# Optimization experiments

Hardware: AMD Instinct MI355X
Metric: run time of the kernel (lower is better)

The kernel has to match this reference:

```python
import jax, jax.numpy as jnp
import numpy as np

EPS = 1e-5

def _bn(x, g, b, m, v):
    # eval-mode batchnorm, NCHW, per-channel params
    inv = g / jnp.sqrt(v + EPS)
    return x * inv[None, :, None, None] + (b - m * inv)[None, :, None, None]

def setup_inputs() -> dict:
    key = jax.random.key(0)
    ks = jax.random.split(key, 16)
    C = 64
    x = jax.random.normal(ks[0], (8, C, 64, 64), dtype=jnp.float32)
    w1 = jax.random.normal(ks[1], (C, C, 1, 1), dtype=jnp.float32) * 0.1
    w2 = jax.random.normal(ks[2], (C, 1, 3, 3), dtype=jnp.float32) * 0.1
    w3 = jax.random.normal(ks[3], (C, C, 1, 1), dtype=jnp.float32) * 0.1
    def bn_params(k):
        k1, k2, k3, k4 = jax.random.split(k, 4)
        return (jax.random.uniform(k1, (C,)) + 0.5,
                jax.random.normal(k2, (C,)) * 0.1,
                jax.random.normal(k3, (C,)) * 0.1,
                jax.random.uniform(k4, (C,)) + 0.5)
    g1, b1, m1, v1 = bn_params(ks[4])
    g2, b2, m2, v2 = bn_params(ks[5])
    g3, b3, m3, v3 = bn_params(ks[6])
    return {"x": x, "w1": w1, "bn1_g": g1, "bn1_b": b1, "bn1_m": m1, "bn1_v": v1,
            "w2": w2, "bn2_g": g2, "bn2_b": b2, "bn2_m": m2, "bn2_v": v2,
            "w3": w3, "bn3_g": g3, "bn3_b": b3, "bn3_m": m3, "bn3_v": v3}

def reference(x, w1, bn1_g, bn1_b, bn1_m, bn1_v,
              w2, bn2_g, bn2_b, bn2_m, bn2_v,
              w3, bn3_g, bn3_b, bn3_m, bn3_v):
    B, c, h, w = x.shape
    N = h * w
    # conv1 (1x1) + BN + ReLU -> V
    v = jnp.einsum('bchw,oc->bohw', x, w1[:, :, 0, 0])
    v = jax.nn.relu(_bn(v, bn1_g, bn1_b, bn1_m, bn1_v))
    # attention over spatial positions: Q=K=x, single head, dim=c
    Q = x.reshape(B, c, N)          # bdn
    V = v.reshape(B, c, N)          # bdm
    scores = jnp.einsum('bdn,bdm->bnm', Q, Q) / (c ** 0.5)  # [B,N,N]
    prob = jax.nn.softmax(scores, axis=-1)
    out = jnp.einsum('bnm,bdm->bdn', prob, V).reshape(B, c, h, w)
    # depthwise conv + BN + ReLU
    out = jax.lax.conv_general_dilated(
        out, w2, window_strides=(1, 1), padding='SAME',
        dimension_numbers=('NCHW', 'OIHW', 'NCHW'), feature_group_count=c)
    out = jax.nn.relu(_bn(out, bn2_g, bn2_b, bn2_m, bn2_v))
    # pointwise conv + BN
    out = jnp.einsum('bchw,oc->bohw', out, w3[:, :, 0, 0])
    out = _bn(out, bn3_g, bn3_b, bn3_m, bn3_v)
    # residual (stride==1 and in_size==out_size)
    return out + x
```

## Files before the change

kernel.cpp:

```cpp
#include <hip/hip_runtime.h>
#include <stdint.h>

typedef __attribute__((ext_vector_type(8)))  short s16x8;
typedef __attribute__((ext_vector_type(16))) float f32x16;

union CvtI4 { int4 i; s16x8 s; };

__device__ __forceinline__ unsigned f2bf(float f) {
    union { float f; unsigned u; } v; v.f = f;
    return (v.u + 0x7fffu + ((v.u >> 16) & 1u)) >> 16;
}

__global__ __launch_bounds__(256) void k_prep(
    const float* __restrict__ x, const float* __restrict__ w1,
    const float* __restrict__ g1, const float* __restrict__ b1,
    const float* __restrict__ m1, const float* __restrict__ v1,
    unsigned short* __restrict__ xT, unsigned short* __restrict__ vbf)
{
    __shared__ float X[64 * 65];
    const int b    = blockIdx.x >> 7;
    const int n0   = ((blockIdx.x >> 1) & 63) << 6;
    const int half = blockIdx.x & 1;
    const int tid  = threadIdx.x;
    const float QS = 0.42466090014400953f;

    {
        const int r = tid >> 6, nn = tid & 63;
        const float* xb = x + (size_t)b * 262144 + n0 + nn;
#pragma unroll
        for (int cc = 0; cc < 16; ++cc) {
            int c = cc * 4 + r;
            X[c * 65 + nn] = xb[(size_t)c * 4096];
        }
    }
    __syncthreads();

    {
        const int n8 = tid >> 3, c8 = tid & 7;
        const int n = (half << 5) + n8;
        unsigned u[4];
#pragma unroll
        for (int j = 0; j < 4; ++j) {
            unsigned lo = f2bf(X[(c8 * 8 + 2 * j) * 65 + n] * QS);
            unsigned hi = f2bf(X[(c8 * 8 + 2 * j + 1) * 65 + n] * QS);
            u[j] = lo | (hi << 16);
        }
        uint4 pk; pk.x = u[0]; pk.y = u[1]; pk.z = u[2]; pk.w = u[3];
        *(uint4*)(xT + (((size_t)((b << 12) + n0 + n)) << 6) + (c8 << 3)) = pk;
    }

    {
        const int n = tid & 63, og = tid >> 6;
        float rX[64];
#pragma unroll
        for (int c = 0; c < 64; ++c) rX[c] = X[c * 65 + n];
        unsigned short* vb = vbf + (((size_t)(b << 6)) << 12) + n0 + n;
#pragma unroll 2
        for (int oo = 0; oo < 8; ++oo) {
            int o = (half << 5) + og * 8 + oo;
            float inv = g1[o] * rsqrtf(v1[o] + 1e-5f);
            float sh  = b1[o] - m1[o] * inv;
            float acc = 0.f;
#pragma unroll
            for (int c = 0; c < 64; ++c) acc = fmaf(w1[o * 64 + c], rX[c], acc);
            vb[(size_t)o << 12] = (unsigned short)f2bf(fmaxf(fmaf(acc, inv, sh), 0.f));
        }
    }
}

__global__ __launch_bounds__(256) void k_attn(
    const unsigned short* __restrict__ xT, const unsigned short* __restrict__ vbf,
    float* __restrict__ outO, float* __restrict__ outL,
    int tilesPer, int nsplit)
{
    __shared__ __align__(16) unsigned short Klds[64 * 64];
    __shared__ __align__(16) unsigned short Vlds[64 * 64];
    __shared__ __align__(16) unsigned short Plds[64 * 64];
    __shared__ float rsLds[4][32];
    __shared__ float denomT[64];

    const int xcd  = blockIdx.x & 7;
    const int slot = blockIdx.x >> 3;
    const int qgrp = slot & 63;
    const int pair = xcd * nsplit + (slot >> 6);
    const int b = pair & 7;
    const int ms = pair >> 3;

    const int tid = threadIdx.x;
    const int w = tid >> 6, lane = tid & 63;
    const int l31 = lane & 31, half = lane >> 5;
    const int qbase = qgrp << 6;

    outO += (size_t)ms * 2097152u;
    outL += (size_t)ms * 32768u;

    const int s = w & 1;
    const int t = w >> 1;

    s16x8 Bq[4];
    {
        const unsigned short* qr = xT +
            (((size_t)((b << 12) + qbase + (t << 5) + l31)) << 6) + (half << 3);
#pragma unroll
        for (int kk = 0; kk < 4; ++kk) {
            CvtI4 c; c.i = *(const int4*)(qr + (kk << 4));
            Bq[kk] = c.s;
        }
    }

    f32x16 O = {0.f,0.f,0.f,0.f,0.f,0.f,0.f,0.f,0.f,0.f,0.f,0.f,0.f,0.f,0.f,0.f};
    float rs = 0.f;
    const int mt0 = ms * tilesPer;

    for (int mt = 0; mt < tilesPer; ++mt) {
        const int m0 = (mt0 + mt) << 6;
        __syncthreads();
#pragma unroll
        for (int it = 0; it < 2; ++it) {
            int lin = (it << 8) + tid;
            {
                int km = lin >> 3, c4 = lin & 7;
                int4 d = *(const int4*)(xT + (((size_t)((b << 12) + m0 + km)) << 6) + (c4 << 3));
                *(int4*)(Klds + (km << 6) + ((c4 ^ (km & 7)) << 3)) = d;
            }
            {
                int vd = lin >> 3, c8 = lin & 7;
                int4 d = *(const int4*)(vbf + (((size_t)((b << 6) + vd)) << 12) + m0 + (c8 << 3));
                *(int4*)(Vlds + (vd << 6) + ((c8 ^ (vd & 7)) << 3)) = d;
            }
        }
        __syncthreads();

        {
            const int km = (s << 5) + l31;
            s16x8 Ak[4];
#pragma unroll
            for (int kk = 0; kk < 4; ++kk) {
                int pos = ((kk << 1) + half) ^ (km & 7);
                Ak[kk] = *(const s16x8*)(Klds + (km << 6) + (pos << 3));
            }
            f32x16 S = {0.f,0.f,0.f,0.f,0.f,0.f,0.f,0.f,0.f,0.f,0.f,0.f,0.f,0.f,0.f,0.f};
            S = __builtin_amdgcn_mfma_f32_32x32x16_bf16(Ak[0], Bq[0], S, 0, 0, 0);
            S = __builtin_amdgcn_mfma_f32_32x32x16_bf16(Ak[1], Bq[1], S, 0, 0, 0);
            S = __builtin_amdgcn_mfma_f32_32x32x16_bf16(Ak[2], Bq[2], S, 0, 0, 0);
            S = __builtin_amdgcn_mfma_f32_32x32x16_bf16(Ak[3], Bq[3], S, 0, 0, 0);

            const int nrow = (t << 5) + l31;
#pragma unroll
            for (int q = 0; q < 4; ++q) {
                float p0 = __builtin_amdgcn_exp2f(S[4*q+0]);
                float p1 = __builtin_amdgcn_exp2f(S[4*q+1]);
                float p2 = __builtin_amdgcn_exp2f(S[4*q+2]);
                float p3 = __builtin_amdgcn_exp2f(S[4*q+3]);
                rs += (p0 + p1) + (p2 + p3);
                union { float f; unsigned u; } a0, a1, a2, a3;
                a0.f = p0; a1.f = p1; a2.f = p2; a3.f = p3;
                uint2 pk;
                pk.x = ((a0.u + 0x8000u) >> 16) | ((a1.u + 0x8000u) & 0xFFFF0000u);
                pk.y = ((a2.u + 0x8000u) >> 16) | ((a3.u + 0x8000u) & 0xFFFF0000u);
                int c8 = (s << 2) + q;
                *(uint2*)(Plds + (nrow << 6) + ((c8 ^ (nrow & 7)) << 3) + (half << 2)) = pk;
            }
        }
        __syncthreads();

        {
            const int nrow = (t << 5) + l31;
            const int drow = (s << 5) + l31;
#pragma unroll
            for (int ks = 0; ks < 4; ++ks) {
                int c = (ks << 1) + half;
                const s16x8 Ap = *(const s16x8*)(Plds + (nrow << 6) + ((c ^ (nrow & 7)) << 3));
                const s16x8 Bv = *(const s16x8*)(Vlds + (drow << 6) + ((c ^ (drow & 7)) << 3));
                O = __builtin_amdgcn_mfma_f32_32x32x16_bf16(Ap, Bv, O, 0, 0, 0);
            }
        }
    }

    rs += __shfl_xor(rs, 32);
    if (half == 0) rsLds[w][l31] = rs;
    __syncthreads();
    if (tid < 64) {
        int tt = tid >> 5, n = tid & 31;
        denomT[tid] = rsLds[2 * tt][n] + rsLds[2 * tt + 1][n];
    }
    __syncthreads();

    const int nb = (b << 12) + qbase;
    const int n32o = w >> 1, d32 = w & 1;
    if (nsplit == 1) {
#pragma unroll
        for (int r = 0; r < 16; ++r) {
            int nl = (r & 3) + ((r >> 2) << 3) + (half << 2);
            int n = (n32o << 5) + nl;
            float inv = 1.f / denomT[n];
            outO[((size_t)(nb + n) << 6) + (d32 << 5) + l31] = O[r] * inv;
        }
    } else {
#pragma unroll
        for (int r = 0; r < 16; ++r) {
            int nl = (r & 3) + ((r >> 2) << 3) + (half << 2);
            int n = (n32o << 5) + nl;
            outO[((size_t)(nb + n) << 6) + (d32 << 5) + l31] = O[r];
        }
        if (tid < 64) outL[nb + tid] = denomT[tid];
    }
}

__global__ __launch_bounds__(256) void k_post(
    const float* __restrict__ Obase, const float* __restrict__ Lbase,
    const float* __restrict__ x,
    const float* __restrict__ w2,
    const float* __restrict__ g2, const float* __restrict__ b2,
    const float* __restrict__ m2, const float* __restrict__ v2,
    const float* __restrict__ w3,
    const float* __restrict__ g3, const float* __restrict__ b3,
    const float* __restrict__ m3, const float* __restrict__ v3,
    float* __restrict__ out, int nsplit, int normalized)
{
    __shared__ float W[3][64 * 66];
    __shared__ float T2[64 * 66];

    const int b = blockIdx.x >> 6;
    const int h = blockIdx.x & 63;
    const int tid = threadIdx.x;

#pragma unroll
    for (int r = 0; r < 3; ++r) {
        int hh = h + r - 1;
        if (hh >= 0 && hh <= 63) {
#pragma unroll
            for (int i = 0; i < 4; ++i) {
                int lin = (i << 8) + tid;
                int w = lin >> 4, cg = lin & 15;
                size_t npos = (size_t)((b << 12) + (hh << 6) + w);
                const float* p0 = Obase + (npos << 6) + (cg << 2);
                float4 a = *(const float4*)p0;
                float sl = normalized ? 0.f : Lbase[npos];
                for (int s = 1; s < nsplit; ++s) {
                    const float4 a2 = *(const float4*)(p0 + (size_t)s * 2097152);
                    a.x += a2.x; a.y += a2.y; a.z += a2.z; a.w += a2.w;
                    sl += Lbase[npos + (size_t)s * 32768];
                }
                float invd = normalized ? 1.f : 1.f / sl;
                a.x *= invd; a.y *= invd; a.z *= invd; a.w *= invd;
                *(float4*)&W[r][w * 66 + (cg << 2)] = a;
            }
        } else {
            float4 z = {0.f, 0.f, 0.f, 0.f};
#pragma unroll
            for (int i = 0; i < 4; ++i) {
                int lin = (i << 8) + tid;
                *(float4*)&W[r][(lin >> 4) * 66 + ((lin & 15) << 2)] = z;
            }
        }
    }
    __syncthreads();

    const int w = tid & 63, cq = tid >> 6;
    float t16[16];
#pragma unroll
    for (int i = 0; i < 16; ++i) t16[i] = 0.f;

#pragma unroll
    for (int ky = 0; ky < 3; ++ky) {
#pragma unroll
        for (int kx = 0; kx < 3; ++kx) {
            int ww = w + kx - 1;
            if (ww < 0 || ww > 63) continue;
            const int k = ky * 3 + kx;
            const float* Wr = &W[ky][ww * 66 + (cq << 4)];
#pragma unroll
            for (int i = 0; i < 4; ++i) {
                float4 a = *(const float4*)(Wr + (i << 2));
                int c = (cq << 4) + (i << 2);
                t16[i * 4 + 0] = fmaf(w2[(c + 0) * 9 + k], a.x, t16[i * 4 + 0]);
                t16[i * 4 + 1] = fmaf(w2[(c + 1) * 9 + k], a.y, t16[i * 4 + 1]);
                t16[i * 4 + 2] = fmaf(w2[(c + 2) * 9 + k], a.z, t16[i * 4 + 2]);
                t16[i * 4 + 3] = fmaf(w2[(c + 3) * 9 + k], a.w, t16[i * 4 + 3]);
            }
        }
    }
#pragma unroll
    for (int i = 0; i < 16; ++i) {
        int c = (cq << 4) + i;
        float inv = g2[c] * rsqrtf(v2[c] + 1e-5f);
        float sh  = b2[c] - m2[c] * inv;
        T2[w * 66 + c] = fmaxf(fmaf(t16[i], inv, sh), 0.f);
    }
    __syncthreads();

    float rT[64];
#pragma unroll
    for (int c4 = 0; c4 < 16; ++c4)
        *(float4*)&rT[c4 << 2] = *(const float4*)&T2[w * 66 + (c4 << 2)];

    const int hw = (h << 6) + w;
#pragma unroll 2
    for (int oo = 0; oo < 16; ++oo) {
        int o = (cq << 4) + oo;
        float inv = g3[o] * rsqrtf(v3[o] + 1e-5f);
        float sh  = b3[o] - m3[o] * inv;
        float acc = 0.f;
#pragma unroll
        for (int c = 0; c < 64; ++c) acc = fmaf(w3[o * 64 + c], rT[c], acc);
        size_t idx = (((size_t)((b << 6) + o)) << 12) + hw;
        out[idx] = fmaf(acc, inv, sh) + x[idx];
    }
}

extern "C" void kernel_launch(void* const* d_in, const int* in_sizes, int n_in,
                              void* d_out, int out_size, void* d_ws, size_t ws_size,
                              hipStream_t stream)
{
    const float* x  = (const float*)d_in[0];
    const float* w1 = (const float*)d_in[1];
    const float* g1 = (const float*)d_in[2];
    const float* b1 = (const float*)d_in[3];
    const float* m1 = (const float*)d_in[4];
    const float* v1 = (const float*)d_in[5];
    const float* w2 = (const float*)d_in[6];
    const float* g2 = (const float*)d_in[7];
    const float* b2 = (const float*)d_in[8];
    const float* m2 = (const float*)d_in[9];
    const float* v2 = (const float*)d_in[10];
    const float* w3 = (const float*)d_in[11];
    const float* g3 = (const float*)d_in[12];
    const float* b3 = (const float*)d_in[13];
    const float* m3 = (const float*)d_in[14];
    const float* v3 = (const float*)d_in[15];
    float* out = (float*)d_out;

    unsigned short* xT  = (unsigned short*)d_ws;
    unsigned short* vbf = xT + (size_t)8 * 4096 * 64;
    float* Obase = (float*)((char*)d_ws + (8u << 20));

    const size_t need2 = (8u << 20) + 2u * ((8u << 20) + (128u << 10));
    const int nsplit = (ws_size >= need2) ? 2 : 1;
    float* Lbase = Obase + (size_t)nsplit * 2097152;

    k_prep<<<1024, 256, 0, stream>>>(x, w1, g1, b1, m1, v1, xT, vbf);
    k_attn<<<nsplit * 512, 256, 0, stream>>>(xT, vbf, Obase, Lbase,
                                             64 / nsplit, nsplit);
    k_post<<<512, 256, 0, stream>>>(Obase, Lbase, x, w2, g2, b2, m2, v2,
                                    w3, g3, b3, m3, v3, out, nsplit, nsplit == 1);
}
```

Baseline: 198.3 us.

## Store attention partials in bf16 and allow four-way key split

The attention kernel now writes its partial output accumulators as bf16 instead of fp32, halving the intermediate buffer traffic. The post kernel reads the partials as packed bf16, converts them back to fp32 and sums across splits. Because each split's buffer is smaller, the workspace can now fit a four-way split of the key dimension, which launches twice as many attention blocks for more parallelism. The cost is reduced precision in the unnormalized partial sums and more partials to merge.

```diff
diff --git a/kernel.cpp b/kernel.cpp
--- a/kernel.cpp
+++ b/kernel.cpp
@@ -70,7 +70,7 @@
 
 __global__ __launch_bounds__(256) void k_attn(
     const unsigned short* __restrict__ xT, const unsigned short* __restrict__ vbf,
-    float* __restrict__ outO, float* __restrict__ outL,
+    unsigned short* __restrict__ outO, float* __restrict__ outL,
     int tilesPer, int nsplit)
 {
     __shared__ __align__(16) unsigned short Klds[64 * 64];
@@ -194,21 +194,21 @@
             int nl = (r & 3) + ((r >> 2) << 3) + (half << 2);
             int n = (n32o << 5) + nl;
             float inv = 1.f / denomT[n];
-            outO[((size_t)(nb + n) << 6) + (d32 << 5) + l31] = O[r] * inv;
+            outO[((size_t)(nb + n) << 6) + (d32 << 5) + l31] = (unsigned short)f2bf(O[r] * inv);
         }
     } else {
 #pragma unroll
         for (int r = 0; r < 16; ++r) {
             int nl = (r & 3) + ((r >> 2) << 3) + (half << 2);
             int n = (n32o << 5) + nl;
-            outO[((size_t)(nb + n) << 6) + (d32 << 5) + l31] = O[r];
+            outO[((size_t)(nb + n) << 6) + (d32 << 5) + l31] = (unsigned short)f2bf(O[r]);
         }
         if (tid < 64) outL[nb + tid] = denomT[tid];
     }
 }
 
 __global__ __launch_bounds__(256) void k_post(
-    const float* __restrict__ Obase, const float* __restrict__ Lbase,
+    const unsigned short* __restrict__ Obase, const float* __restrict__ Lbase,
     const float* __restrict__ x,
     const float* __restrict__ w2,
     const float* __restrict__ g2, const float* __restrict__ b2,
@@ -230,28 +230,40 @@
         int hh = h + r - 1;
         if (hh >= 0 && hh <= 63) {
 #pragma unroll
-            for (int i = 0; i < 4; ++i) {
+            for (int i = 0; i < 2; ++i) {
                 int lin = (i << 8) + tid;
-                int w = lin >> 4, cg = lin & 15;
+                int w = lin >> 3, cg = lin & 7;
                 size_t npos = (size_t)((b << 12) + (hh << 6) + w);
-                const float* p0 = Obase + (npos << 6) + (cg << 2);
-                float4 a = *(const float4*)p0;
+                float acc[8];
+#pragma unroll
+                for (int j = 0; j < 8; ++j) acc[j] = 0.f;
                 float sl = normalized ? 0.f : Lbase[npos];
-                for (int s = 1; s < nsplit; ++s) {
-                    const float4 a2 = *(const float4*)(p0 + (size_t)s * 2097152);
-                    a.x += a2.x; a.y += a2.y; a.z += a2.z; a.w += a2.w;
-                    sl += Lbase[npos + (size_t)s * 32768];
+                const unsigned short* p0 = Obase + (npos << 6) + (cg << 3);
+                for (int s = 0; s < nsplit; ++s) {
+                    uint4 v = *(const uint4*)(p0 + (size_t)s * 2097152u);
+                    union { float f; unsigned u; } t;
+                    t.u = v.x << 16;        acc[0] += t.f;
+                    t.u = v.x & 0xFFFF0000u; acc[1] += t.f;
+                    t.u = v.y << 16;        acc[2] += t.f;
+                    t.u = v.y & 0xFFFF0000u; acc[3] += t.f;
+                    t.u = v.z << 16;        acc[4] += t.f;
+                    t.u = v.z & 0xFFFF0000u; acc[5] += t.f;
+                    t.u = v.w << 16;        acc[6] += t.f;
+                    t.u = v.w & 0xFFFF0000u; acc[7] += t.f;
+                    if (s && !normalized) sl += Lbase[npos + (size_t)s * 32768u];
                 }
                 float invd = normalized ? 1.f : 1.f / sl;
-                a.x *= invd; a.y *= invd; a.z *= invd; a.w *= invd;
-                *(float4*)&W[r][w * 66 + (cg << 2)] = a;
+                float* Wd = &W[r][w * 66 + (cg << 3)];
+#pragma unroll
+                for (int j = 0; j < 8; ++j) Wd[j] = acc[j] * invd;
             }
         } else {
-            float4 z = {0.f, 0.f, 0.f, 0.f};
-#pragma unroll
-            for (int i = 0; i < 4; ++i) {
+#pragma unroll
+            for (int i = 0; i < 2; ++i) {
                 int lin = (i << 8) + tid;
-                *(float4*)&W[r][(lin >> 4) * 66 + ((lin & 15) << 2)] = z;
+                float* Wd = &W[r][(lin >> 3) * 66 + ((lin & 7) << 3)];
+#pragma unroll
+                for (int j = 0; j < 8; ++j) Wd[j] = 0.f;
             }
         }
     }
@@ -333,11 +345,12 @@
 
     unsigned short* xT  = (unsigned short*)d_ws;
     unsigned short* vbf = xT + (size_t)8 * 4096 * 64;
-    float* Obase = (float*)((char*)d_ws + (8u << 20));
-
-    const size_t need2 = (8u << 20) + 2u * ((8u << 20) + (128u << 10));
-    const int nsplit = (ws_size >= need2) ? 2 : 1;
-    float* Lbase = Obase + (size_t)nsplit * 2097152;
+    unsigned short* Obase = (unsigned short*)((char*)d_ws + (8u << 20));
+
+    const size_t need4 = (8u << 20) + 4u * ((4u << 20) + (128u << 10));
+    const size_t need2 = (8u << 20) + 2u * ((4u << 20) + (128u << 10));
+    const int nsplit = (ws_size >= need4) ? 4 : (ws_size >= need2 ? 2 : 1);
+    float* Lbase = (float*)(Obase + (size_t)nsplit * 2097152u);
 
     k_prep<<<1024, 256, 0, stream>>>(x, w1, g1, b1, m1, v1, xT, vbf);
     k_attn<<<nsplit * 512, 256, 0, stream>>>(xT, vbf, Obase, Lbase,
```

Result: slower. 203.2 us (+2.5%).
